# Kernel optimization log

Measured on AMD Instinct MI355X. Metric: run time of the kernel, lower is better.

Reference implementation:

```python
import jax, jax.numpy as jnp
import numpy as np

B, S, D, H = 4, 2048, 1024, 16
Dh = D // H


def _layernorm(x, a, b):
    # torch.var default is unbiased (ddof=1)
    mu = jnp.mean(x, axis=-1, keepdims=True)
    sg = jnp.var(x, axis=-1, keepdims=True, ddof=1)
    return (x - mu) / jnp.sqrt(sg + 1e-08) * a + b


def setup_inputs() -> dict:
    key = jax.random.key(0)
    ks = jax.random.split(key, 16)
    s = 1.0 / np.sqrt(D)
    inp = {
        'q': jax.random.normal(ks[0], (B, S, D), jnp.float32),
        'k': jax.random.normal(ks[1], (B, S, D), jnp.float32),
        'v': jax.random.normal(ks[2], (B, S, D), jnp.float32),
        'g': jax.random.normal(ks[3], (B, S, D), jnp.float32),
        # causal mask: True = masked
        'm': jnp.triu(jnp.ones((S, S), jnp.bool_), k=1)[None, None],
        'Wq': jax.random.uniform(ks[4], (D, D), jnp.float32, -s, s),
        'bq': jnp.zeros((D,), jnp.float32),
        'Wk': jax.random.uniform(ks[5], (D, D), jnp.float32, -s, s),
        'bk': jnp.zeros((D,), jnp.float32),
        'Wv': jax.random.uniform(ks[6], (D, D), jnp.float32, -s, s),
        'bv': jnp.zeros((D,), jnp.float32),
        'Wg': jax.random.uniform(ks[7], (D, D), jnp.float32, -s, s),
        'bg': jnp.zeros((D,), jnp.float32),
        'ln_a': jnp.ones((D,), jnp.float32),
        'ln_b': jnp.zeros((D,), jnp.float32),
        'Wo': jax.random.uniform(ks[8], (D, D), jnp.float32, -s, s),
        'bo': jnp.zeros((D,), jnp.float32),
    }
    return inp


def reference(q, k, v, g, m, Wq, bq, Wk, bk, Wv, bv, Wg, bg, ln_a, ln_b, Wo, bo):
    qp = q @ Wq.T + bq
    kp = k @ Wk.T + bk
    vp = v @ Wv.T + bv
    gp = g @ Wg.T + bg
    # gating path: exact GELU (torch default), then custom LayerNorm (unbiased var)
    vp = jax.nn.gelu(vp, approximate=False)
    gp = jax.nn.gelu(gp, approximate=False)
    vp = _layernorm(vp, ln_a, ln_b)
    # [B,S,D] -> [B,H,S,Dh]
    qh = qp.reshape(B, S, H, Dh).transpose(0, 2, 1, 3)
    kh = kp.reshape(B, S, H, Dh).transpose(0, 2, 1, 3)
    vh = vp.reshape(B, S, H, Dh).transpose(0, 2, 1, 3)
    gh = gp.reshape(B, S, H, Dh).transpose(0, 2, 1, 3)
    a = jnp.einsum('bhqd,bhkd->bhqk', qh, kh) / jnp.sqrt(jnp.float32(Dh))
    a = jnp.where(m, -jnp.inf, a)
    a = jax.nn.softmax(a, axis=-1)
    # dropout = 0.0 (inference): no-op
    o = jnp.einsum('bhqk,bhkd->bhqd', a, vh)
    o = o * gh
    o = o.transpose(0, 2, 1, 3).reshape(B, S, D)
    o = o @ Wo.T + bo
    return (o, a)
```

## Files before the change

kernel.cpp:

```cpp
#include <hip/hip_runtime.h>
#include <hip/hip_bf16.h>
#include <cstdint>
#include <cstddef>

#define DEVINL static __device__ __forceinline__

typedef short bf16x8 __attribute__((ext_vector_type(8)));
typedef short s16x4  __attribute__((ext_vector_type(4)));
typedef float f32x4  __attribute__((ext_vector_type(4)));
typedef unsigned short u16;

static constexpr int Bb = 4, Ss = 2048, Dd = 1024, Hh = 16;
static constexpr int Mrows = Bb * Ss;
static constexpr int BHc = Bb * Hh;

DEVINL u16 f2bf(float f) {
    union { float f; uint32_t u; } v; v.f = f;
    uint32_t r = v.u + 0x7fffu + ((v.u >> 16) & 1u);
    return (u16)(r >> 16);
}
DEVINL float bf2f(u16 h) {
    union { uint32_t u; float f; } v; v.u = ((uint32_t)h) << 16;
    return v.f;
}
DEVINL uint32_t cvt_pk_bf16(float lo, float hi) {
    uint32_t r;
    asm("v_cvt_pk_bf16_f32 %0, %1, %2" : "=v"(r) : "v"(lo), "v"(hi));
    return r;
}
DEVINL float gelu_exact(float x) {
    return 0.5f * x * (1.0f + erff(x * 0.70710678118654752f));
}
DEVINL void gload16(const u16* gsrc, u16* ldsdst) {
    auto* g = reinterpret_cast<const __attribute__((address_space(1))) uint32_t*>(
        reinterpret_cast<uintptr_t>(gsrc));
    auto* l = reinterpret_cast<__attribute__((address_space(3))) uint32_t*>(
        reinterpret_cast<uintptr_t>(ldsdst));
    __builtin_amdgcn_global_load_lds(g, l, 16, 0, 0);
}

__global__ __launch_bounds__(256) void k_cvt_in(
    const float* __restrict__ s0, const float* __restrict__ s1,
    const float* __restrict__ s2, const float* __restrict__ s3,
    u16* __restrict__ d0, u16* __restrict__ d1,
    u16* __restrict__ d2, u16* __restrict__ d3, int n4) {
    int t = blockIdx.x * 256 + threadIdx.x;
    if (t >= n4) return;
    const float* s; u16* d;
    switch (blockIdx.y) {
        case 0: s = s0; d = d0; break;
        case 1: s = s1; d = d1; break;
        case 2: s = s2; d = d2; break;
        default: s = s3; d = d3; break;
    }
    float4 v = ((const float4*)s)[t];
    ushort4 o;
    o.x = f2bf(v.x); o.y = f2bf(v.y); o.z = f2bf(v.z); o.w = f2bf(v.w);
    ((ushort4*)d)[t] = o;
}

__global__ __launch_bounds__(256) void k_cvt_w(
    const float* __restrict__ s0, const float* __restrict__ s1,
    const float* __restrict__ s2, const float* __restrict__ s3,
    const float* __restrict__ s4,
    u16* __restrict__ d0, u16* __restrict__ d1, u16* __restrict__ d2,
    u16* __restrict__ d3, u16* __restrict__ d4, int n4) {
    int t = blockIdx.x * 256 + threadIdx.x;
    if (t >= n4) return;
    const float* s; u16* d;
    switch (blockIdx.y) {
        case 0: s = s0; d = d0; break;
        case 1: s = s1; d = d1; break;
        case 2: s = s2; d = d2; break;
        case 3: s = s3; d = d3; break;
        default: s = s4; d = d4; break;
    }
    float4 v = ((const float4*)s)[t];
    ushort4 o;
    o.x = f2bf(v.x); o.y = f2bf(v.y); o.z = f2bf(v.z); o.w = f2bf(v.w);
    ((ushort4*)d)[t] = o;
}

__global__ __launch_bounds__(256) void k_proj(
    const u16* __restrict__ qb, const u16* __restrict__ kb,
    const u16* __restrict__ vb, const u16* __restrict__ gb,
    const u16* __restrict__ Wqb, const u16* __restrict__ Wkb,
    const u16* __restrict__ Wvb, const u16* __restrict__ Wgb,
    const float* __restrict__ bqp, const float* __restrict__ bkp,
    const float* __restrict__ bvp, const float* __restrict__ bgp,
    u16* __restrict__ qp, u16* __restrict__ kpo,
    float* __restrict__ vp, u16* __restrict__ ghb)
{
    __shared__ u16 As[128 * 32];
    __shared__ u16 Bs[128 * 32];
    const int tid = threadIdx.x, lane = tid & 63, w = tid >> 6;
    const int wm = w >> 1, wn = w & 1;
    const int g = lane >> 4, li = lane & 15;
    const int orig = blockIdx.x;
    const int lid = (orig & 7) * 256 + (orig >> 3);
    const int z = lid >> 9, rem = lid & 511;
    const int m0 = (rem >> 3) * 128, n0 = (rem & 7) * 128;

    const u16 *Ap, *Wp; const float* bias;
    switch (z) {
        case 0: Ap = qb; Wp = Wqb; bias = bqp; break;
        case 1: Ap = kb; Wp = Wkb; bias = bkp; break;
        case 2: Ap = vb; Wp = Wvb; bias = bvp; break;
        default: Ap = gb; Wp = Wgb; bias = bgp; break;
    }

    const f32x4 zero4 = {0.f, 0.f, 0.f, 0.f};
    f32x4 acc[4][4];
#pragma unroll
    for (int m = 0; m < 4; m++)
#pragma unroll
        for (int n = 0; n < 4; n++) acc[m][n] = zero4;

    for (int k0 = 0; k0 < 1024; k0 += 32) {
        __syncthreads();
#pragma unroll
        for (int i = 0; i < 2; i++) {
            int chunk = (w * 2 + i) * 64 + lane;
            int row = chunk >> 2, cp = chunk & 3;
            gload16(Ap + (size_t)(m0 + row) * 1024 + k0 + ((cp ^ ((row >> 1) & 3)) << 3),
                    &As[(w * 2 + i) * 512]);
        }
#pragma unroll
        for (int i = 0; i < 2; i++) {
            int chunk = (w * 2 + i) * 64 + lane;
            int row = chunk >> 2, cp = chunk & 3;
            gload16(Wp + (size_t)(n0 + row) * 1024 + k0 + ((cp ^ ((row >> 1) & 3)) << 3),
                    &Bs[(w * 2 + i) * 512]);
        }
        __syncthreads();

        bf16x8 af[4], bfr[4];
#pragma unroll
        for (int m = 0; m < 4; m++) {
            int row = wm * 64 + m * 16 + li;
            af[m] = *(const bf16x8*)&As[row * 32 + ((g ^ ((row >> 1) & 3)) << 3)];
        }
#pragma unroll
        for (int n = 0; n < 4; n++) {
            int row = wn * 64 + n * 16 + li;
            bfr[n] = *(const bf16x8*)&Bs[row * 32 + ((g ^ ((row >> 1) & 3)) << 3)];
        }
#pragma unroll
        for (int m = 0; m < 4; m++)
#pragma unroll
            for (int n = 0; n < 4; n++)
                acc[m][n] = __builtin_amdgcn_mfma_f32_16x16x32_bf16(af[m], bfr[n], acc[m][n], 0, 0, 0);
    }

#pragma unroll
    for (int m = 0; m < 4; m++) {
#pragma unroll
        for (int n = 0; n < 4; n++) {
            int col = n0 + wn * 64 + n * 16 + li;
            float bv = bias[col];
#pragma unroll
            for (int r = 0; r < 4; r++) {
                int row = m0 + wm * 64 + m * 16 + g * 4 + r;
                float v = acc[m][n][r] + bv;
                size_t idx = (size_t)row * 1024 + col;
                if (z == 0)      qp[idx]  = f2bf(v * 0.125f);
                else if (z == 1) kpo[idx] = f2bf(v);
                else if (z == 2) vp[idx]  = gelu_exact(v);
                else             ghb[idx] = f2bf(gelu_exact(v));
            }
        }
    }
}

__global__ __launch_bounds__(256) void k_gemm_f(
    const u16* __restrict__ Ap, const u16* __restrict__ Wp,
    const float* __restrict__ bias, float* __restrict__ Cp)
{
    __shared__ u16 As[128 * 32];
    __shared__ u16 Bs[128 * 32];
    const int tid = threadIdx.x, lane = tid & 63, w = tid >> 6;
    const int wm = w >> 1, wn = w & 1;
    const int g = lane >> 4, li = lane & 15;
    const int orig = blockIdx.x;
    const int lid = (orig & 7) * 64 + (orig >> 3);
    const int m0 = (lid >> 3) * 128, n0 = (lid & 7) * 128;

    const f32x4 zero4 = {0.f, 0.f, 0.f, 0.f};
    f32x4 acc[4][4];
#pragma unroll
    for (int m = 0; m < 4; m++)
#pragma unroll
        for (int n = 0; n < 4; n++) acc[m][n] = zero4;

    for (int k0 = 0; k0 < 1024; k0 += 32) {
        __syncthreads();
#pragma unroll
        for (int i = 0; i < 2; i++) {
            int chunk = (w * 2 + i) * 64 + lane;
            int row = chunk >> 2, cp = chunk & 3;
            gload16(Ap + (size_t)(m0 + row) * 1024 + k0 + ((cp ^ ((row >> 1) & 3)) << 3),
                    &As[(w * 2 + i) * 512]);
        }
#pragma unroll
        for (int i = 0; i < 2; i++) {
            int chunk = (w * 2 + i) * 64 + lane;
            int row = chunk >> 2, cp = chunk & 3;
            gload16(Wp + (size_t)(n0 + row) * 1024 + k0 + ((cp ^ ((row >> 1) & 3)) << 3),
                    &Bs[(w * 2 + i) * 512]);
        }
        __syncthreads();

        bf16x8 af[4], bfr[4];
#pragma unroll
        for (int m = 0; m < 4; m++) {
            int row = wm * 64 + m * 16 + li;
            af[m] = *(const bf16x8*)&As[row * 32 + ((g ^ ((row >> 1) & 3)) << 3)];
        }
#pragma unroll
        for (int n = 0; n < 4; n++) {
            int row = wn * 64 + n * 16 + li;
            bfr[n] = *(const bf16x8*)&Bs[row * 32 + ((g ^ ((row >> 1) & 3)) << 3)];
        }
#pragma unroll
        for (int m = 0; m < 4; m++)
#pragma unroll
            for (int n = 0; n < 4; n++)
                acc[m][n] = __builtin_amdgcn_mfma_f32_16x16x32_bf16(af[m], bfr[n], acc[m][n], 0, 0, 0);
    }

#pragma unroll
    for (int m = 0; m < 4; m++) {
#pragma unroll
        for (int n = 0; n < 4; n++) {
            int col = n0 + wn * 64 + n * 16 + li;
            float bv = bias[col];
#pragma unroll
            for (int r = 0; r < 4; r++) {
                int row = m0 + wm * 64 + m * 16 + g * 4 + r;
                Cp[(size_t)row * 1024 + col] = acc[m][n][r] + bv;
            }
        }
    }
}

__global__ __launch_bounds__(256) void k_ln(const float* __restrict__ vp,
                                            const float* __restrict__ la,
                                            const float* __restrict__ lb,
                                            u16* __restrict__ vh) {
    int row = blockIdx.x;
    const float* x = vp + (size_t)row * 1024;
    int tid = threadIdx.x;
    float4 v = ((const float4*)x)[tid];
    float s = v.x + v.y + v.z + v.w;
    float s2 = v.x * v.x + v.y * v.y + v.z * v.z + v.w * v.w;
#pragma unroll
    for (int off = 1; off < 64; off <<= 1) {
        s  += __shfl_xor(s, off, 64);
        s2 += __shfl_xor(s2, off, 64);
    }
    __shared__ float red[8];
    int w = tid >> 6, lane = tid & 63;
    if (lane == 0) { red[w] = s; red[4 + w] = s2; }
    __syncthreads();
    s  = red[0] + red[1] + red[2] + red[3];
    s2 = red[4] + red[5] + red[6] + red[7];
    float mu = s * (1.0f / 1024.0f);
    float var = (s2 - 1024.0f * mu * mu) * (1.0f / 1023.0f);
    float rs = rsqrtf(var + 1e-8f);
    float4 a4 = ((const float4*)la)[tid];
    float4 b4 = ((const float4*)lb)[tid];
    ushort4 o;
    o.x = f2bf((v.x - mu) * rs * a4.x + b4.x);
    o.y = f2bf((v.y - mu) * rs * a4.y + b4.y);
    o.z = f2bf((v.z - mu) * rs * a4.z + b4.z);
    o.w = f2bf((v.w - mu) * rs * a4.w + b4.w);
    ((ushort4*)(vh + (size_t)row * 1024))[tid] = o;
}

__global__ __launch_bounds__(256) void k_transpose(const u16* __restrict__ vh,
                                                   u16* __restrict__ vhT) {
    int bh = blockIdx.y, b = bh >> 4, h = bh & 15, s0 = blockIdx.x * 64;
    __shared__ u16 t[64 * 96];
    int tid = threadIdx.x;
#pragma unroll
    for (int j = 0; j < 2; j++) {
        int u = j * 256 + tid;
        int r = u >> 3, c8 = u & 7;
        bf16x8 v = *(const bf16x8*)(vh + ((size_t)(b * 2048 + s0 + r) * 1024 + h * 64 + c8 * 8));
        *(bf16x8*)&t[r * 96 + c8 * 8] = v;
    }
    __syncthreads();
#pragma unroll
    for (int j = 0; j < 2; j++) {
        int u = j * 256 + tid;
        int d = u >> 3, s8 = u & 7;
        bf16x8 vv;
#pragma unroll
        for (int jj = 0; jj < 8; jj++) vv[jj] = (short)t[(s8 * 8 + jj) * 96 + d];
        *(bf16x8*)(vhT + ((size_t)(bh * 64 + d) * 2048 + s0 + s8 * 8)) = vv;
    }
}

__global__ __launch_bounds__(512) void k_attn(const u16* __restrict__ qp,
                                              const u16* __restrict__ kp,
                                              const u16* __restrict__ vhT,
                                              const u16* __restrict__ gh,
                                              float* __restrict__ aout,
                                              u16* __restrict__ gated) {
    __shared__ short Ps[8 * 16 * 128];
    const int tid = threadIdx.x, lane = tid & 63, w = tid >> 6;
    const int g = lane >> 4, li = lane & 15;
    const int orig = blockIdx.x;
    const int lid = (orig & 7) * 64 + (orig >> 3);
    const int bh = lid >> 3, i0 = lid & 7;
    const int b = bh >> 4, h = bh & 15;
    const u16* kbh = kp + ((size_t)(b * 2048) * 1024 + h * 64);
    const u16* vbh = vhT + (size_t)bh * 64 * 2048;
    const u16* ghb_base = gh + (size_t)(b * 2048) * 1024 + h * 64;
    float* arow = aout + (size_t)bh * 2048 * 2048;
    short* Pw = &Ps[w * 2048];
    const f32x4 zero4 = {0.f, 0.f, 0.f, 0.f};

    for (int half = 0; half < 2; ++half) {
        const int bx = half ? (15 - i0) : i0;
        const int q0 = bx * 128;
        const int qrow0 = q0 + w * 16;
        const int qrow = qrow0 + li;
        const u16* qbase = qp + ((size_t)(b * 2048 + qrow) * 1024 + h * 64 + g * 8);
        bf16x8 qa0 = *(const bf16x8*)qbase;
        bf16x8 qa1 = *(const bf16x8*)(qbase + 32);

        for (int kt = bx + 1; kt < 16; ++kt) {
            float* tbase = arow + (size_t)q0 * 2048 + kt * 128;
#pragma unroll
            for (int i = 0; i < 8; i++) {
                int u = i * 512 + tid;
                int row = u >> 5, cu = u & 31;
                __builtin_nontemporal_store(zero4, (f32x4*)(tbase + (size_t)row * 2048 + cu * 4));
            }
        }

        float l_run = 0.f;
        for (int kt = 0; kt <= bx; ++kt) {
            const int k0 = kt * 128;
            const bool full = (kt < bx);
#pragma unroll
            for (int n = 0; n < 8; n++) {
                int rb = k0 + n * 16 + li;
                const u16* krow = kbh + (size_t)rb * 1024 + g * 8;
                bf16x8 kb0 = *(const bf16x8*)krow;
                bf16x8 kb1 = *(const bf16x8*)(krow + 32);
                f32x4 c = zero4;
                c = __builtin_amdgcn_mfma_f32_16x16x32_bf16(kb0, qa0, c, 0, 0, 0);
                c = __builtin_amdgcn_mfma_f32_16x16x32_bf16(kb1, qa1, c, 0, 0, 0);
                if (full) {
#pragma unroll
                    for (int r = 0; r < 4; r++) l_run += __expf(c[r]);
                } else {
#pragma unroll
                    for (int r = 0; r < 4; r++) {
                        int col = k0 + n * 16 + g * 4 + r;
                        l_run += (col <= qrow) ? __expf(c[r]) : 0.0f;
                    }
                }
            }
        }
        l_run += __shfl_xor(l_run, 16, 64);
        l_run += __shfl_xor(l_run, 32, 64);
        const float linv = 1.0f / l_run;

        f32x4 oacc[4];
#pragma unroll
        for (int n = 0; n < 4; n++) oacc[n] = zero4;
        for (int kt = 0; kt <= bx; ++kt) {
            const int k0 = kt * 128;
            const bool full = (kt < bx);
#pragma unroll
            for (int n = 0; n < 8; n++) {
                int rb = k0 + n * 16 + li;
                const u16* krow = kbh + (size_t)rb * 1024 + g * 8;
                bf16x8 kb0 = *(const bf16x8*)krow;
                bf16x8 kb1 = *(const bf16x8*)(krow + 32);
                f32x4 c = zero4;
                c = __builtin_amdgcn_mfma_f32_16x16x32_bf16(kb0, qa0, c, 0, 0, 0);
                c = __builtin_amdgcn_mfma_f32_16x16x32_bf16(kb1, qa1, c, 0, 0, 0);
                if (full) {
#pragma unroll
                    for (int r = 0; r < 4; r++) c[r] = __expf(c[r]) * linv;
                } else {
#pragma unroll
                    for (int r = 0; r < 4; r++) {
                        int col = k0 + n * 16 + g * 4 + r;
                        c[r] = (col <= qrow) ? __expf(c[r]) * linv : 0.0f;
                    }
                }
                __builtin_nontemporal_store(c,
                    (f32x4*)(arow + (size_t)qrow * 2048 + k0 + n * 16 + g * 4));
                uint2 pk;
                pk.x = cvt_pk_bf16(c[0], c[1]);
                pk.y = cvt_pk_bf16(c[2], c[3]);
                int chunk = n * 2 + (g >> 1);
                *(uint2*)&Pw[li * 128 + ((chunk ^ (li & 7)) << 3) + (g & 1) * 4] = pk;
            }
#pragma unroll
            for (int ks = 0; ks < 4; ++ks) {
                int cl = ks * 4 + g;
                bf16x8 pa = *(const bf16x8*)&Pw[li * 128 + ((cl ^ (li & 7)) << 3)];
#pragma unroll
                for (int n = 0; n < 4; n++) {
                    int vr = n * 16 + li;
                    bf16x8 vb = *(const bf16x8*)(vbh + (size_t)vr * 2048 + k0 + cl * 8);
                    oacc[n] = __builtin_amdgcn_mfma_f32_16x16x32_bf16(pa, vb, oacc[n], 0, 0, 0);
                }
            }
        }

#pragma unroll
        for (int n = 0; n < 4; n++) {
            int d8 = n * 2 + (li >> 3), wi = li & 7;
#pragma unroll
            for (int r = 0; r < 4; r++) {
                int lr = g * 4 + r;
                Pw[lr * 64 + ((d8 ^ (lr & 7)) << 3) + wi] = (short)f2bf(oacc[n][r]);
            }
        }
#pragma unroll
        for (int it = 0; it < 2; ++it) {
            int lr = it * 8 + (lane >> 3);
            int c8 = lane & 7;
            int rowq = qrow0 + lr;
            bf16x8 ov = *(const bf16x8*)&Pw[lr * 64 + ((c8 ^ (lr & 7)) << 3)];
            bf16x8 gv = *(const bf16x8*)(ghb_base + (size_t)rowq * 1024 + c8 * 8);
            float p0 = bf2f((u16)ov[0]) * bf2f((u16)gv[0]);
            float p1 = bf2f((u16)ov[1]) * bf2f((u16)gv[1]);
            float p2 = bf2f((u16)ov[2]) * bf2f((u16)gv[2]);
            float p3 = bf2f((u16)ov[3]) * bf2f((u16)gv[3]);
            float p4 = bf2f((u16)ov[4]) * bf2f((u16)gv[4]);
            float p5 = bf2f((u16)ov[5]) * bf2f((u16)gv[5]);
            float p6 = bf2f((u16)ov[6]) * bf2f((u16)gv[6]);
            float p7 = bf2f((u16)ov[7]) * bf2f((u16)gv[7]);
            uint4 outv;
            outv.x = cvt_pk_bf16(p0, p1);
            outv.y = cvt_pk_bf16(p2, p3);
            outv.z = cvt_pk_bf16(p4, p5);
            outv.w = cvt_pk_bf16(p6, p7);
            *(uint4*)(gated + ((size_t)(b * 2048 + rowq)) * 1024 + h * 64 + c8 * 8) = outv;
        }
    }
}

extern "C" void kernel_launch(void* const* d_in, const int* in_sizes, int n_in,
                              void* d_out, int out_size, void* d_ws, size_t ws_size,
                              hipStream_t stream) {
    const float* q  = (const float*)d_in[0];
    const float* k  = (const float*)d_in[1];
    const float* v  = (const float*)d_in[2];
    const float* g  = (const float*)d_in[3];
    const float* Wq = (const float*)d_in[5];
    const float* bq = (const float*)d_in[6];
    const float* Wk = (const float*)d_in[7];
    const float* bk = (const float*)d_in[8];
    const float* Wv = (const float*)d_in[9];
    const float* bv = (const float*)d_in[10];
    const float* Wg = (const float*)d_in[11];
    const float* bg = (const float*)d_in[12];
    const float* ln_a = (const float*)d_in[13];
    const float* ln_b = (const float*)d_in[14];
    const float* Wo = (const float*)d_in[15];
    const float* bo = (const float*)d_in[16];

    float* o_out = (float*)d_out;
    float* a_out = o_out + (size_t)Mrows * Dd;

    u16* qp    = (u16*)d_ws;
    u16* kpb   = qp    + (size_t)Mrows * Dd;
    u16* vhT   = kpb   + (size_t)Mrows * Dd;
    u16* ghb   = vhT   + (size_t)Mrows * Dd;
    u16* gated = ghb   + (size_t)Mrows * Dd;
    u16* Wo_bf = gated + (size_t)Mrows * Dd;

    u16* Wq_bf = (u16*)a_out;
    u16* Wk_bf = Wq_bf + (size_t)Dd * Dd;
    u16* Wv_bf = Wk_bf + (size_t)Dd * Dd;
    u16* Wg_bf = Wv_bf + (size_t)Dd * Dd;
    u16* qb    = Wg_bf + (size_t)Dd * Dd;
    u16* kb2   = qb    + (size_t)Mrows * Dd;
    u16* vb    = kb2   + (size_t)Mrows * Dd;
    u16* gb    = vb    + (size_t)Mrows * Dd;
    float* vp  = (float*)(gb + (size_t)Mrows * Dd);
    u16* vh    = (u16*)(vp + (size_t)Mrows * Dd);

    {
        int n4w = Dd * Dd / 4;
        dim3 gw((n4w + 255) / 256, 5);
        k_cvt_w<<<gw, 256, 0, stream>>>(Wq, Wk, Wv, Wg, Wo,
                                        Wq_bf, Wk_bf, Wv_bf, Wg_bf, Wo_bf, n4w);
        int n4i = Mrows * Dd / 4;
        dim3 gi((n4i + 255) / 256, 4);
        k_cvt_in<<<gi, 256, 0, stream>>>(q, k, v, g, qb, kb2, vb, gb, n4i);
    }

    k_proj<<<2048, 256, 0, stream>>>(qb, kb2, vb, gb,
                                     Wq_bf, Wk_bf, Wv_bf, Wg_bf,
                                     bq, bk, bv, bg,
                                     qp, kpb, vp, ghb);

    k_ln<<<Mrows, 256, 0, stream>>>(vp, ln_a, ln_b, vh);

    dim3 gt(Ss / 64, BHc);
    k_transpose<<<gt, 256, 0, stream>>>(vh, vhT);

    k_attn<<<512, 512, 0, stream>>>(qp, kpb, vhT, ghb, a_out, gated);

    k_gemm_f<<<512, 256, 0, stream>>>(gated, Wo_bf, bo, o_out);
}
```

Measured before the change: 676.6 us.

## Enlarge projection and output GEMM tiles to 256x256x64 with 8 waves

```diff
diff --git a/kernel.cpp b/kernel.cpp
--- a/kernel.cpp
+++ b/kernel.cpp
@@ -81,7 +81,7 @@
     ((ushort4*)d)[t] = o;
 }
 
-__global__ __launch_bounds__(256) void k_proj(
+__global__ __launch_bounds__(512) void k_proj(
     const u16* __restrict__ qb, const u16* __restrict__ kb,
     const u16* __restrict__ vb, const u16* __restrict__ gb,
     const u16* __restrict__ Wqb, const u16* __restrict__ Wkb,
@@ -91,15 +91,15 @@
     u16* __restrict__ qp, u16* __restrict__ kpo,
     float* __restrict__ vp, u16* __restrict__ ghb)
 {
-    __shared__ u16 As[128 * 32];
-    __shared__ u16 Bs[128 * 32];
+    __shared__ u16 As[256 * 64];
+    __shared__ u16 Bs[256 * 64];
     const int tid = threadIdx.x, lane = tid & 63, w = tid >> 6;
-    const int wm = w >> 1, wn = w & 1;
+    const int wm = w >> 2, wn = w & 3;
     const int g = lane >> 4, li = lane & 15;
     const int orig = blockIdx.x;
-    const int lid = (orig & 7) * 256 + (orig >> 3);
-    const int z = lid >> 9, rem = lid & 511;
-    const int m0 = (rem >> 3) * 128, n0 = (rem & 7) * 128;
+    const int lid = (orig & 7) * 64 + (orig >> 3);
+    const int z = lid >> 7, rem = lid & 127;
+    const int m0 = (rem >> 2) * 256, n0 = (rem & 3) * 256;
 
     const u16 *Ap, *Wp; const float* bias;
     switch (z) {
@@ -110,58 +110,63 @@
     }
 
     const f32x4 zero4 = {0.f, 0.f, 0.f, 0.f};
-    f32x4 acc[4][4];
-#pragma unroll
-    for (int m = 0; m < 4; m++)
-#pragma unroll
-        for (int n = 0; n < 4; n++) acc[m][n] = zero4;
-
-    for (int k0 = 0; k0 < 1024; k0 += 32) {
+    f32x4 acc[8][4];
+#pragma unroll
+    for (int mi = 0; mi < 8; mi++)
+#pragma unroll
+        for (int ni = 0; ni < 4; ni++) acc[mi][ni] = zero4;
+
+    for (int k0 = 0; k0 < 1024; k0 += 64) {
         __syncthreads();
 #pragma unroll
-        for (int i = 0; i < 2; i++) {
-            int chunk = (w * 2 + i) * 64 + lane;
-            int row = chunk >> 2, cp = chunk & 3;
-            gload16(Ap + (size_t)(m0 + row) * 1024 + k0 + ((cp ^ ((row >> 1) & 3)) << 3),
-                    &As[(w * 2 + i) * 512]);
-        }
-#pragma unroll
-        for (int i = 0; i < 2; i++) {
-            int chunk = (w * 2 + i) * 64 + lane;
-            int row = chunk >> 2, cp = chunk & 3;
-            gload16(Wp + (size_t)(n0 + row) * 1024 + k0 + ((cp ^ ((row >> 1) & 3)) << 3),
-                    &Bs[(w * 2 + i) * 512]);
+        for (int i = 0; i < 4; i++) {
+            int u = i * 512 + w * 64 + lane;
+            int row = u >> 3, cp = u & 7;
+            gload16(Ap + (size_t)(m0 + row) * 1024 + k0 + ((cp ^ (row & 7)) << 3),
+                    &As[(i * 512 + w * 64) * 8]);
+        }
+#pragma unroll
+        for (int i = 0; i < 4; i++) {
+            int u = i * 512 + w * 64 + lane;
+            int row = u >> 3, cp = u & 7;
+            gload16(Wp + (size_t)(n0 + row) * 1024 + k0 + ((cp ^ (row & 7)) << 3),
+                    &Bs[(i * 512 + w * 64) * 8]);
         }
         __syncthreads();
 
-        bf16x8 af[4], bfr[4];
-#pragma unroll
-        for (int m = 0; m < 4; m++) {
-            int row = wm * 64 + m * 16 + li;
-            af[m] = *(const bf16x8*)&As[row * 32 + ((g ^ ((row >> 1) & 3)) << 3)];
-        }
-#pragma unroll
-        for (int n = 0; n < 4; n++) {
-            int row = wn * 64 + n * 16 + li;
-            bfr[n] = *(const bf16x8*)&Bs[row * 32 + ((g ^ ((row >> 1) & 3)) << 3)];
-        }
-#pragma unroll
-        for (int m = 0; m < 4; m++)
-#pragma unroll
-            for (int n = 0; n < 4; n++)
-                acc[m][n] = __builtin_amdgcn_mfma_f32_16x16x32_bf16(af[m], bfr[n], acc[m][n], 0, 0, 0);
-    }
-
-#pragma unroll
-    for (int m = 0; m < 4; m++) {
-#pragma unroll
-        for (int n = 0; n < 4; n++) {
-            int col = n0 + wn * 64 + n * 16 + li;
+#pragma unroll
+        for (int kk2 = 0; kk2 < 2; kk2++) {
+            bf16x8 af[8], bfr[4];
+#pragma unroll
+            for (int mi = 0; mi < 8; mi++) {
+                int row = wm * 128 + mi * 16 + li;
+                int lc = kk2 * 4 + g;
+                af[mi] = *(const bf16x8*)&As[row * 64 + ((lc ^ (row & 7)) << 3)];
+            }
+#pragma unroll
+            for (int ni = 0; ni < 4; ni++) {
+                int row = wn * 64 + ni * 16 + li;
+                int lc = kk2 * 4 + g;
+                bfr[ni] = *(const bf16x8*)&Bs[row * 64 + ((lc ^ (row & 7)) << 3)];
+            }
+#pragma unroll
+            for (int mi = 0; mi < 8; mi++)
+#pragma unroll
+                for (int ni = 0; ni < 4; ni++)
+                    acc[mi][ni] = __builtin_amdgcn_mfma_f32_16x16x32_bf16(af[mi], bfr[ni], acc[mi][ni], 0, 0, 0);
+        }
+    }
+
+#pragma unroll
+    for (int mi = 0; mi < 8; mi++) {
+#pragma unroll
+        for (int ni = 0; ni < 4; ni++) {
+            int col = n0 + wn * 64 + ni * 16 + li;
             float bv = bias[col];
 #pragma unroll
             for (int r = 0; r < 4; r++) {
-                int row = m0 + wm * 64 + m * 16 + g * 4 + r;
-                float v = acc[m][n][r] + bv;
+                int row = m0 + wm * 128 + mi * 16 + g * 4 + r;
+                float v = acc[mi][ni][r] + bv;
                 size_t idx = (size_t)row * 1024 + col;
                 if (z == 0)      qp[idx]  = f2bf(v * 0.125f);
                 else if (z == 1) kpo[idx] = f2bf(v);
@@ -172,72 +177,77 @@
     }
 }
 
-__global__ __launch_bounds__(256) void k_gemm_f(
+__global__ __launch_bounds__(512) void k_gemm_f(
     const u16* __restrict__ Ap, const u16* __restrict__ Wp,
     const float* __restrict__ bias, float* __restrict__ Cp)
 {
-    __shared__ u16 As[128 * 32];
-    __shared__ u16 Bs[128 * 32];
+    __shared__ u16 As[256 * 64];
+    __shared__ u16 Bs[256 * 64];
     const int tid = threadIdx.x, lane = tid & 63, w = tid >> 6;
-    const int wm = w >> 1, wn = w & 1;
+    const int wm = w >> 2, wn = w & 3;
     const int g = lane >> 4, li = lane & 15;
     const int orig = blockIdx.x;
-    const int lid = (orig & 7) * 64 + (orig >> 3);
-    const int m0 = (lid >> 3) * 128, n0 = (lid & 7) * 128;
+    const int lid = (orig & 7) * 16 + (orig >> 3);
+    const int m0 = (lid >> 2) * 256, n0 = (lid & 3) * 256;
 
     const f32x4 zero4 = {0.f, 0.f, 0.f, 0.f};
-    f32x4 acc[4][4];
-#pragma unroll
-    for (int m = 0; m < 4; m++)
-#pragma unroll
-        for (int n = 0; n < 4; n++) acc[m][n] = zero4;
-
-    for (int k0 = 0; k0 < 1024; k0 += 32) {
+    f32x4 acc[8][4];
+#pragma unroll
+    for (int mi = 0; mi < 8; mi++)
+#pragma unroll
+        for (int ni = 0; ni < 4; ni++) acc[mi][ni] = zero4;
+
+    for (int k0 = 0; k0 < 1024; k0 += 64) {
         __syncthreads();
 #pragma unroll
-        for (int i = 0; i < 2; i++) {
-            int chunk = (w * 2 + i) * 64 + lane;
-            int row = chunk >> 2, cp = chunk & 3;
-            gload16(Ap + (size_t)(m0 + row) * 1024 + k0 + ((cp ^ ((row >> 1) & 3)) << 3),
-                    &As[(w * 2 + i) * 512]);
-        }
-#pragma unroll
-        for (int i = 0; i < 2; i++) {
-            int chunk = (w * 2 + i) * 64 + lane;
-            int row = chunk >> 2, cp = chunk & 3;
-            gload16(Wp + (size_t)(n0 + row) * 1024 + k0 + ((cp ^ ((row >> 1) & 3)) << 3),
-                    &Bs[(w * 2 + i) * 512]);
+        for (int i = 0; i < 4; i++) {
+            int u = i * 512 + w * 64 + lane;
+            int row = u >> 3, cp = u & 7;
+            gload16(Ap + (size_t)(m0 + row) * 1024 + k0 + ((cp ^ (row & 7)) << 3),
+                    &As[(i * 512 + w * 64) * 8]);
+        }
+#pragma unroll
+        for (int i = 0; i < 4; i++) {
+            int u = i * 512 + w * 64 + lane;
+            int row = u >> 3, cp = u & 7;
+            gload16(Wp + (size_t)(n0 + row) * 1024 + k0 + ((cp ^ (row & 7)) << 3),
+                    &Bs[(i * 512 + w * 64) * 8]);
         }
         __syncthreads();
 
-        bf16x8 af[4], bfr[4];
-#pragma unroll
-        for (int m = 0; m < 4; m++) {
-            int row = wm * 64 + m * 16 + li;
-            af[m] = *(const bf16x8*)&As[row * 32 + ((g ^ ((row >> 1) & 3)) << 3)];
-        }
-#pragma unroll
-        for (int n = 0; n < 4; n++) {
-            int row = wn * 64 + n * 16 + li;
-            bfr[n] = *(const bf16x8*)&Bs[row * 32 + ((g ^ ((row >> 1) & 3)) << 3)];
-        }
-#pragma unroll
-        for (int m = 0; m < 4; m++)
-#pragma unroll
-            for (int n = 0; n < 4; n++)
-                acc[m][n] = __builtin_amdgcn_mfma_f32_16x16x32_bf16(af[m], bfr[n], acc[m][n], 0, 0, 0);
-    }
-
-#pragma unroll
-    for (int m = 0; m < 4; m++) {
-#pragma unroll
-        for (int n = 0; n < 4; n++) {
-            int col = n0 + wn * 64 + n * 16 + li;
+#pragma unroll
+        for (int kk2 = 0; kk2 < 2; kk2++) {
+            bf16x8 af[8], bfr[4];
+#pragma unroll
+            for (int mi = 0; mi < 8; mi++) {
+                int row = wm * 128 + mi * 16 + li;
+                int lc = kk2 * 4 + g;
+                af[mi] = *(const bf16x8*)&As[row * 64 + ((lc ^ (row & 7)) << 3)];
+            }
+#pragma unroll
+            for (int ni = 0; ni < 4; ni++) {
+                int row = wn * 64 + ni * 16 + li;
+                int lc = kk2 * 4 + g;
+                bfr[ni] = *(const bf16x8*)&Bs[row * 64 + ((lc ^ (row & 7)) << 3)];
+            }
+#pragma unroll
+            for (int mi = 0; mi < 8; mi++)
+#pragma unroll
+                for (int ni = 0; ni < 4; ni++)
+                    acc[mi][ni] = __builtin_amdgcn_mfma_f32_16x16x32_bf16(af[mi], bfr[ni], acc[mi][ni], 0, 0, 0);
+        }
+    }
+
+#pragma unroll
+    for (int mi = 0; mi < 8; mi++) {
+#pragma unroll
+        for (int ni = 0; ni < 4; ni++) {
+            int col = n0 + wn * 64 + ni * 16 + li;
             float bv = bias[col];
 #pragma unroll
             for (int r = 0; r < 4; r++) {
-                int row = m0 + wm * 64 + m * 16 + g * 4 + r;
-                Cp[(size_t)row * 1024 + col] = acc[m][n][r] + bv;
+                int row = m0 + wm * 128 + mi * 16 + g * 4 + r;
+                Cp[(size_t)row * 1024 + col] = acc[mi][ni][r] + bv;
             }
         }
     }
@@ -500,10 +510,10 @@
         k_cvt_in<<<gi, 256, 0, stream>>>(q, k, v, g, qb, kb2, vb, gb, n4i);
     }
 
-    k_proj<<<2048, 256, 0, stream>>>(qb, kb2, vb, gb,
-                                     Wq_bf, Wk_bf, Wv_bf, Wg_bf,
-                                     bq, bk, bv, bg,
-                                     qp, kpb, vp, ghb);
+    k_proj<<<512, 512, 0, stream>>>(qb, kb2, vb, gb,
+                                    Wq_bf, Wk_bf, Wv_bf, Wg_bf,
+                                    bq, bk, bv, bg,
+                                    qp, kpb, vp, ghb);
 
     k_ln<<<Mrows, 256, 0, stream>>>(vp, ln_a, ln_b, vh);
 
@@ -512,5 +522,5 @@
 
     k_attn<<<512, 512, 0, stream>>>(qp, kpb, vhT, ghb, a_out, gated);
 
-    k_gemm_f<<<512, 256, 0, stream>>>(gated, Wo_bf, bo, o_out);
-}
+    k_gemm_f<<<128, 512, 0, stream>>>(gated, Wo_bf, bo, o_out);
+}
```

Result: slower. 721.3 us (+6.6%).

## Load GEMM fragments directly from global memory, dropping LDS staging

Applied to the files above, without the earlier changes.

```diff
diff --git a/kernel.cpp b/kernel.cpp
--- a/kernel.cpp
+++ b/kernel.cpp
@@ -30,13 +30,6 @@
 }
 DEVINL float gelu_exact(float x) {
     return 0.5f * x * (1.0f + erff(x * 0.70710678118654752f));
-}
-DEVINL void gload16(const u16* gsrc, u16* ldsdst) {
-    auto* g = reinterpret_cast<const __attribute__((address_space(1))) uint32_t*>(
-        reinterpret_cast<uintptr_t>(gsrc));
-    auto* l = reinterpret_cast<__attribute__((address_space(3))) uint32_t*>(
-        reinterpret_cast<uintptr_t>(ldsdst));
-    __builtin_amdgcn_global_load_lds(g, l, 16, 0, 0);
 }
 
 __global__ __launch_bounds__(256) void k_cvt_in(
@@ -91,8 +84,6 @@
     u16* __restrict__ qp, u16* __restrict__ kpo,
     float* __restrict__ vp, u16* __restrict__ ghb)
 {
-    __shared__ u16 As[128 * 32];
-    __shared__ u16 Bs[128 * 32];
     const int tid = threadIdx.x, lane = tid & 63, w = tid >> 6;
     const int wm = w >> 1, wn = w & 1;
     const int g = lane >> 4, li = lane & 15;
@@ -109,6 +100,9 @@
         default: Ap = gb; Wp = Wgb; bias = bgp; break;
     }
 
+    const u16* Abase = Ap + (size_t)(m0 + wm * 64 + li) * 1024 + g * 8;
+    const u16* Wbase = Wp + (size_t)(n0 + wn * 64 + li) * 1024 + g * 8;
+
     const f32x4 zero4 = {0.f, 0.f, 0.f, 0.f};
     f32x4 acc[4][4];
 #pragma unroll
@@ -116,35 +110,15 @@
 #pragma unroll
         for (int n = 0; n < 4; n++) acc[m][n] = zero4;
 
+#pragma unroll 2
     for (int k0 = 0; k0 < 1024; k0 += 32) {
-        __syncthreads();
-#pragma unroll
-        for (int i = 0; i < 2; i++) {
-            int chunk = (w * 2 + i) * 64 + lane;
-            int row = chunk >> 2, cp = chunk & 3;
-            gload16(Ap + (size_t)(m0 + row) * 1024 + k0 + ((cp ^ ((row >> 1) & 3)) << 3),
-                    &As[(w * 2 + i) * 512]);
-        }
-#pragma unroll
-        for (int i = 0; i < 2; i++) {
-            int chunk = (w * 2 + i) * 64 + lane;
-            int row = chunk >> 2, cp = chunk & 3;
-            gload16(Wp + (size_t)(n0 + row) * 1024 + k0 + ((cp ^ ((row >> 1) & 3)) << 3),
-                    &Bs[(w * 2 + i) * 512]);
-        }
-        __syncthreads();
-
         bf16x8 af[4], bfr[4];
 #pragma unroll
-        for (int m = 0; m < 4; m++) {
-            int row = wm * 64 + m * 16 + li;
-            af[m] = *(const bf16x8*)&As[row * 32 + ((g ^ ((row >> 1) & 3)) << 3)];
-        }
-#pragma unroll
-        for (int n = 0; n < 4; n++) {
-            int row = wn * 64 + n * 16 + li;
-            bfr[n] = *(const bf16x8*)&Bs[row * 32 + ((g ^ ((row >> 1) & 3)) << 3)];
-        }
+        for (int m = 0; m < 4; m++)
+            af[m] = *(const bf16x8*)(Abase + (size_t)(m * 16) * 1024 + k0);
+#pragma unroll
+        for (int n = 0; n < 4; n++)
+            bfr[n] = *(const bf16x8*)(Wbase + (size_t)(n * 16) * 1024 + k0);
 #pragma unroll
         for (int m = 0; m < 4; m++)
 #pragma unroll
@@ -176,8 +150,6 @@
     const u16* __restrict__ Ap, const u16* __restrict__ Wp,
     const float* __restrict__ bias, float* __restrict__ Cp)
 {
-    __shared__ u16 As[128 * 32];
-    __shared__ u16 Bs[128 * 32];
     const int tid = threadIdx.x, lane = tid & 63, w = tid >> 6;
     const int wm = w >> 1, wn = w & 1;
     const int g = lane >> 4, li = lane & 15;
@@ -185,6 +157,9 @@
     const int lid = (orig & 7) * 64 + (orig >> 3);
     const int m0 = (lid >> 3) * 128, n0 = (lid & 7) * 128;
 
+    const u16* Abase = Ap + (size_t)(m0 + wm * 64 + li) * 1024 + g * 8;
+    const u16* Wbase = Wp + (size_t)(n0 + wn * 64 + li) * 1024 + g * 8;
+
     const f32x4 zero4 = {0.f, 0.f, 0.f, 0.f};
     f32x4 acc[4][4];
 #pragma unroll
@@ -192,35 +167,15 @@
 #pragma unroll
         for (int n = 0; n < 4; n++) acc[m][n] = zero4;
 
+#pragma unroll 2
     for (int k0 = 0; k0 < 1024; k0 += 32) {
-        __syncthreads();
-#pragma unroll
-        for (int i = 0; i < 2; i++) {
-            int chunk = (w * 2 + i) * 64 + lane;
-            int row = chunk >> 2, cp = chunk & 3;
-            gload16(Ap + (size_t)(m0 + row) * 1024 + k0 + ((cp ^ ((row >> 1) & 3)) << 3),
-                    &As[(w * 2 + i) * 512]);
-        }
-#pragma unroll
-        for (int i = 0; i < 2; i++) {
-            int chunk = (w * 2 + i) * 64 + lane;
-            int row = chunk >> 2, cp = chunk & 3;
-            gload16(Wp + (size_t)(n0 + row) * 1024 + k0 + ((cp ^ ((row >> 1) & 3)) << 3),
-                    &Bs[(w * 2 + i) * 512]);
-        }
-        __syncthreads();
-
         bf16x8 af[4], bfr[4];
 #pragma unroll
-        for (int m = 0; m < 4; m++) {
-            int row = wm * 64 + m * 16 + li;
-            af[m] = *(const bf16x8*)&As[row * 32 + ((g ^ ((row >> 1) & 3)) << 3)];
-        }
-#pragma unroll
-        for (int n = 0; n < 4; n++) {
-            int row = wn * 64 + n * 16 + li;
-            bfr[n] = *(const bf16x8*)&Bs[row * 32 + ((g ^ ((row >> 1) & 3)) << 3)];
-        }
+        for (int m = 0; m < 4; m++)
+            af[m] = *(const bf16x8*)(Abase + (size_t)(m * 16) * 1024 + k0);
+#pragma unroll
+        for (int n = 0; n < 4; n++)
+            bfr[n] = *(const bf16x8*)(Wbase + (size_t)(n * 16) * 1024 + k0);
 #pragma unroll
         for (int m = 0; m < 4; m++)
 #pragma unroll
```

After: 860.3 us. 1.27x slower.
